# Performance work log

Measured on AMD Instinct MI355X. Metric: run time of the kernel, lower is better.

## Reference

```python
import jax, jax.numpy as jnp
import numpy as np

B, C, D_IN, D_H, D_OUT = 131072, 16, 256, 1024, 256


def setup_inputs() -> dict:
    key = jax.random.key(0)
    k = jax.random.split(key, 6)
    return {
        "x": jax.random.normal(k[0], (B, D_IN), dtype=jnp.float32),
        "cat_ids": jax.random.randint(k[1], (B,), 0, C, dtype=jnp.int32),
        "W1": jax.random.normal(k[2], (C, D_IN, D_H), dtype=jnp.float32) * (1.0 / np.sqrt(D_IN)),
        "b1": jax.random.normal(k[3], (C, D_H), dtype=jnp.float32) * 0.02,
        "W2": jax.random.normal(k[4], (C, D_H, D_OUT), dtype=jnp.float32) * (1.0 / np.sqrt(D_H)),
        "b2": jax.random.normal(k[5], (C, D_OUT), dtype=jnp.float32) * 0.02,
    }


def _routed_linear(x, cat_ids, W, b):
    # Category-routed linear: out[i] = x[i] @ W[cat_ids[i]] + b[cat_ids[i]].
    # Loop over the small fixed category count (not over tokens); each branch
    # is a dense GEMM masked by the routing assignment. This is equivalent to
    # the original gather -> per-category Linear -> scatter/argsort pattern
    # without materializing per-token weight gathers.
    num_categories = W.shape[0]
    out = jnp.zeros((x.shape[0], W.shape[2]), dtype=x.dtype)
    for c in range(num_categories):
        mask = (cat_ids == c)[:, None]
        out = out + jnp.where(mask, x @ W[c] + b[c], jnp.zeros((), x.dtype))
    return out


def reference(x, cat_ids, W1, b1, W2, b2):
    hidden = jax.nn.relu(_routed_linear(x, cat_ids, W1, b1))
    return _routed_linear(hidden, cat_ids, W2, b2)
```

## Files before the change

### kernel.cpp

```cpp
#include <hip/hip_runtime.h>
#include <hip/hip_bf16.h>

#define BB   131072
#define CC   16
#define DIN  256
#define DH   1024
#define DOUT 256
#define TM   128
#define NHB  32
#define NB   512

typedef __attribute__((ext_vector_type(8))) short bf16x8;
typedef __attribute__((ext_vector_type(4))) short short4v;
typedef __attribute__((ext_vector_type(4))) float f32x4;

__device__ inline unsigned short f2b(float f) {
  union { float f; unsigned u; } v; v.f = f;
  unsigned u = v.u;
  return (unsigned short)((u + 0x7fffu + ((u >> 16) & 1u)) >> 16);
}

__device__ inline void gload_lds16(const void* g, void* l) {
  __builtin_amdgcn_global_load_lds(
      (const __attribute__((address_space(1))) void*)g,
      (__attribute__((address_space(3))) void*)l, 16, 0, 0);
}

#define MFMA16(a, b, c) __builtin_amdgcn_mfma_f32_16x16x32_bf16((a), (b), (c), 0, 0, 0)

__global__ void hist_k(const int* __restrict__ cat, int* __restrict__ blockhist) {
  __shared__ int h[CC];
  const int tid = threadIdx.x;
  if (tid < CC) h[tid] = 0;
  __syncthreads();
  const int i = blockIdx.x * 256 + tid;
  atomicAdd(&h[cat[i]], 1);
  __syncthreads();
  if (tid < CC) blockhist[blockIdx.x * CC + tid] = h[tid];
}

__global__ void offsets2_k(const int* __restrict__ blockhist,
                           int* __restrict__ counts, int* __restrict__ padoff,
                           int* __restrict__ base) {
  __shared__ int part[CC][64];
  __shared__ int pref[CC][64];
  __shared__ int scnt[CC];
  __shared__ int spad[CC + 1];
  const int tid = threadIdx.x;
  const int c = tid >> 6;
  const int g = tid & 63;
  int h[8];
  int s = 0;
#pragma unroll
  for (int i = 0; i < 8; i++) {
    h[i] = blockhist[(g * 8 + i) * CC + c];
    s += h[i];
  }
  part[c][g] = s;
  __syncthreads();
  if (g == 0) {
    int r = 0;
    for (int j = 0; j < 64; j++) { pref[c][j] = r; r += part[c][j]; }
    scnt[c] = r;
  }
  __syncthreads();
  if (tid == 0) {
    int acc = 0;
    for (int c2 = 0; c2 < CC; c2++) {
      spad[c2] = acc;
      padoff[c2] = acc;
      counts[c2] = scnt[c2];
      acc += ((scnt[c2] + TM - 1) / TM) * TM;
    }
    spad[CC] = acc;
    padoff[CC] = acc;
  }
  __syncthreads();
  int run = spad[c] + pref[c][g];
#pragma unroll
  for (int i = 0; i < 8; i++) {
    base[(g * 8 + i) * CC + c] = run;
    run += h[i];
  }
}

__global__ void scatter2_k(const int* __restrict__ cat, const int* __restrict__ base,
                           int* __restrict__ idx) {
  __shared__ int cur[CC];
  const int tid = threadIdx.x;
  if (tid < CC) cur[tid] = base[blockIdx.x * CC + tid];
  __syncthreads();
  const int i = blockIdx.x * 256 + tid;
  const int c = cat[i];
  const int pos = atomicAdd(&cur[c], 1);
  idx[pos] = i;
}

__global__ void conv_w1_k(const float* __restrict__ W1, short* __restrict__ w1b) {
  int t = blockIdx.x * blockDim.x + threadIdx.x;
  int n  = t & 1023;
  int j8 = (t >> 10) & 31;
  int c  = t >> 15;
  const float* src = W1 + (size_t)c * DIN * DH;
  bf16x8 o;
#pragma unroll
  for (int i = 0; i < 8; i++)
    o[i] = (short)f2b(src[(size_t)(j8 * 8 + i) * DH + n]);
  char* dst = (char*)w1b + (size_t)c * 524288
            + (n >> 5) * 16384 + ((n >> 4) & 1) * 8192 + (j8 >> 2) * 1024
            + ((n & 15) + 16 * (j8 & 3)) * 16;
  *(bf16x8*)dst = o;
}

__global__ void conv_w2_k(const float* __restrict__ W2, short* __restrict__ w2b) {
  int t = blockIdx.x * blockDim.x + threadIdx.x;
  int n  = t & 255;
  int j8 = (t >> 8) & 127;
  int c  = t >> 15;
  const float* src = W2 + (size_t)c * DH * DOUT;
  bf16x8 o;
#pragma unroll
  for (int i = 0; i < 8; i++)
    o[i] = (short)f2b(src[(size_t)(j8 * 8 + i) * DOUT + n]);
  char* dst = (char*)w2b + (size_t)c * 524288
            + (j8 >> 2) * 16384 + (n >> 4) * 1024
            + ((n & 15) + 16 * (j8 & 3)) * 16;
  *(bf16x8*)dst = o;
}

#define W2OFF  32768
#define HSOFF  65536
#define TKOFF  81920
#define B1OFF  82432
#define B2OFF  86528
#define SMSZ   87552

__launch_bounds__(512, 2)
__global__ void mlp_k(const float* __restrict__ x,
                      const float* __restrict__ b1,
                      const float* __restrict__ b2,
                      const short* __restrict__ w1b,
                      const short* __restrict__ w2b,
                      const int* __restrict__ idx,
                      const int* __restrict__ padoff,
                      const int* __restrict__ counts,
                      float* __restrict__ out) {
  __shared__ __align__(16) char sm[SMSZ];

  const int bhw = blockIdx.x;
  const int wg = (bhw & 7) * 130 + (bhw >> 3);
  const int p = wg * TM;
  const int total = padoff[CC];
  if (p >= total) return;
  int c = 0;
  while (padoff[c + 1] <= p) c++;
  const int cnt = counts[c];
  const int start = p - padoff[c];

  const int tid  = threadIdx.x;
  const int lane = tid & 63;
  const int w    = tid >> 6;
  const int wt   = w >> 1;
  const int wh   = w & 1;
  const int lrow = lane & 15;
  const int lgrp = lane >> 4;

  char*  hsb   = sm + HSOFF;
  int*   toksp = (int*)(sm + TKOFF);
  float* b1s   = (float*)(sm + B1OFF);
  float* b2s   = (float*)(sm + B2OFF);

  {
    const int r = tid >> 2;
    const int q = tid & 3;
    const int pos = start + r;
    int tok = (pos < cnt) ? idx[p + r] : -1;
    if (q == 0) toksp[r] = tok;
    char* tb = sm + (r >> 4) * 8192 + (r & 15) * 16;
    if (tok >= 0) {
      const f32x4* src = (const f32x4*)(x + (size_t)tok * DIN) + q * 16;
#pragma unroll
      for (int t = 0; t < 8; t++) {
        f32x4 v0 = src[2 * t];
        f32x4 v1 = src[2 * t + 1];
        bf16x8 o;
        o[0] = (short)f2b(v0[0]); o[1] = (short)f2b(v0[1]);
        o[2] = (short)f2b(v0[2]); o[3] = (short)f2b(v0[3]);
        o[4] = (short)f2b(v1[0]); o[5] = (short)f2b(v1[1]);
        o[6] = (short)f2b(v1[2]); o[7] = (short)f2b(v1[3]);
        *(bf16x8*)(tb + (2 * q + (t >> 2)) * 1024 + (t & 3) * 256) = o;
      }
    } else {
      bf16x8 z = {0, 0, 0, 0, 0, 0, 0, 0};
#pragma unroll
      for (int t = 0; t < 8; t++)
        *(bf16x8*)(tb + (2 * q + (t >> 2)) * 1024 + (t & 3) * 256) = z;
    }
    if (tid < 256) ((f32x4*)b1s)[tid] = ((const f32x4*)(b1 + (size_t)c * DH))[tid];
    if (tid < 64)  ((f32x4*)b2s)[tid] = ((const f32x4*)(b2 + (size_t)c * DOUT))[tid];
  }
  __syncthreads();

  bf16x8 xf[2][8];
#pragma unroll
  for (int ti = 0; ti < 2; ti++)
#pragma unroll
    for (int ks = 0; ks < 8; ks++)
      xf[ti][ks] = *(const bf16x8*)(sm + (2 * wt + ti) * 8192 + ks * 1024 + lane * 16);
  __syncthreads();

  const char* w1g = (const char*)w1b + (size_t)c * 524288;
  const char* w2g = (const char*)w2b + (size_t)c * 524288;

  auto stage1 = [&](int i) {
    const char* src = w1g + (size_t)i * 16384;
    char* dst = sm + (i & 1) * 16384;
#pragma unroll
    for (int j = 0; j < 2; j++) {
      int chunk = (w * 2 + j) * 1024;
      gload_lds16(src + chunk + lane * 16, dst + chunk);
    }
  };
  auto stage2 = [&](int i) {
    const char* src = w2g + (size_t)i * 16384;
    char* dst = sm + W2OFF + (i & 1) * 16384;
#pragma unroll
    for (int j = 0; j < 2; j++) {
      int chunk = (w * 2 + j) * 1024;
      gload_lds16(src + chunk + lane * 16, dst + chunk);
    }
  };

  f32x4 acc2[2][8];
#pragma unroll
  for (int ti = 0; ti < 2; ti++)
#pragma unroll
    for (int ni = 0; ni < 8; ni++)
      acc2[ti][ni] = (f32x4){0.f, 0.f, 0.f, 0.f};

  const int hswr = (lrow + 16 * (wh * 2 + (lgrp >> 1))) * 16 + (lgrp & 1) * 8;

  stage1(0);
  asm volatile("s_waitcnt vmcnt(0)" ::: "memory");
  __builtin_amdgcn_s_barrier();

  {
    stage2(0);
    stage1(1);
    const char* w1c = sm + wh * 8192;
    f32x4 p0 = (f32x4){0.f, 0.f, 0.f, 0.f};
    f32x4 p1 = (f32x4){0.f, 0.f, 0.f, 0.f};
    __builtin_amdgcn_s_setprio(1);
#pragma unroll
    for (int ks = 0; ks < 8; ks++) {
      bf16x8 a = *(const bf16x8*)(w1c + ks * 1024 + lane * 16);
      p0 = MFMA16(a, xf[0][ks], p0);
      p1 = MFMA16(a, xf[1][ks], p1);
    }
    __builtin_amdgcn_s_setprio(0);
    f32x4 bv = *(const f32x4*)(b1s + wh * 16 + lgrp * 4);
    short4v h0, h1;
#pragma unroll
    for (int jj = 0; jj < 4; jj++) {
      h0[jj] = (short)f2b(fmaxf(p0[jj] + bv[jj], 0.0f));
      h1[jj] = (short)f2b(fmaxf(p1[jj] + bv[jj], 0.0f));
    }
    *(short4v*)(hsb + (2 * wt) * 1024 + hswr)     = h0;
    *(short4v*)(hsb + (2 * wt + 1) * 1024 + hswr) = h1;
    asm volatile("s_waitcnt vmcnt(0) lgkmcnt(0)" ::: "memory");
    __builtin_amdgcn_s_barrier();
  }

  for (int i = 1; i < NHB; i++) {
    stage2(i);
    if (i < NHB - 1) stage1(i + 1);

    const char* hr  = hsb + ((i - 1) & 1) * 8192;
    const char* w2c = sm + W2OFF + ((i - 1) & 1) * 16384;
    const char* w1c = sm + (i & 1) * 16384 + wh * 8192;

    bf16x8 hf0 = *(const bf16x8*)(hr + (2 * wt) * 1024 + lane * 16);
    bf16x8 hf1 = *(const bf16x8*)(hr + (2 * wt + 1) * 1024 + lane * 16);

    __builtin_amdgcn_s_setprio(1);
#pragma unroll
    for (int ni = 0; ni < 8; ni++) {
      bf16x8 a2 = *(const bf16x8*)(w2c + (wh * 8 + ni) * 1024 + lane * 16);
      acc2[0][ni] = MFMA16(a2, hf0, acc2[0][ni]);
      acc2[1][ni] = MFMA16(a2, hf1, acc2[1][ni]);
    }
    f32x4 p0 = (f32x4){0.f, 0.f, 0.f, 0.f};
    f32x4 p1 = (f32x4){0.f, 0.f, 0.f, 0.f};
#pragma unroll
    for (int ks = 0; ks < 8; ks++) {
      bf16x8 a = *(const bf16x8*)(w1c + ks * 1024 + lane * 16);
      p0 = MFMA16(a, xf[0][ks], p0);
      p1 = MFMA16(a, xf[1][ks], p1);
    }
    __builtin_amdgcn_s_setprio(0);

    f32x4 bv = *(const f32x4*)(b1s + i * 32 + wh * 16 + lgrp * 4);
    short4v h0, h1;
#pragma unroll
    for (int jj = 0; jj < 4; jj++) {
      h0[jj] = (short)f2b(fmaxf(p0[jj] + bv[jj], 0.0f));
      h1[jj] = (short)f2b(fmaxf(p1[jj] + bv[jj], 0.0f));
    }
    char* hw = hsb + (i & 1) * 8192;
    *(short4v*)(hw + (2 * wt) * 1024 + hswr)     = h0;
    *(short4v*)(hw + (2 * wt + 1) * 1024 + hswr) = h1;

    asm volatile("s_waitcnt vmcnt(0) lgkmcnt(0)" ::: "memory");
    __builtin_amdgcn_s_barrier();
  }

  {
    const char* hr  = hsb + ((NHB - 1) & 1) * 8192;
    const char* w2c = sm + W2OFF + ((NHB - 1) & 1) * 16384;
    bf16x8 hf0 = *(const bf16x8*)(hr + (2 * wt) * 1024 + lane * 16);
    bf16x8 hf1 = *(const bf16x8*)(hr + (2 * wt + 1) * 1024 + lane * 16);
#pragma unroll
    for (int ni = 0; ni < 8; ni++) {
      bf16x8 a2 = *(const bf16x8*)(w2c + (wh * 8 + ni) * 1024 + lane * 16);
      acc2[0][ni] = MFMA16(a2, hf0, acc2[0][ni]);
      acc2[1][ni] = MFMA16(a2, hf1, acc2[1][ni]);
    }
  }

#pragma unroll
  for (int ti = 0; ti < 2; ti++) {
    const int tok = toksp[(2 * wt + ti) * 16 + lrow];
    if (tok >= 0) {
#pragma unroll
      for (int ni = 0; ni < 8; ni++) {
        const int n0 = (wh * 8 + ni) * 16 + lgrp * 4;
        f32x4 bv = *(const f32x4*)(b2s + n0);
        f32x4 v = acc2[ti][ni] + bv;
        *(f32x4*)(out + (size_t)tok * DOUT + n0) = v;
      }
    }
  }
}

extern "C" void kernel_launch(void* const* d_in, const int* in_sizes, int n_in,
                              void* d_out, int out_size, void* d_ws, size_t ws_size,
                              hipStream_t stream) {
  (void)in_sizes; (void)n_in; (void)out_size; (void)ws_size;
  const float* x   = (const float*)d_in[0];
  const int*   cat = (const int*)d_in[1];
  const float* W1  = (const float*)d_in[2];
  const float* b1  = (const float*)d_in[3];
  const float* W2  = (const float*)d_in[4];
  const float* b2  = (const float*)d_in[5];
  float* out = (float*)d_out;

  char* ws = (char*)d_ws;
  int* counts    = (int*)(ws);
  int* padoff    = (int*)(ws + 128);
  int* blockhist = (int*)(ws + 4096);
  int* base      = (int*)(ws + 65536);
  int* idx       = (int*)(ws + 131072);
  short* w1b     = (short*)(ws + (1 << 20));
  short* w2b     = (short*)(ws + (1 << 20) + 8388608);

  hist_k<<<NB, 256, 0, stream>>>(cat, blockhist);
  offsets2_k<<<1, 1024, 0, stream>>>(blockhist, counts, padoff, base);
  scatter2_k<<<NB, 256, 0, stream>>>(cat, base, idx);
  conv_w1_k<<<2048, 256, 0, stream>>>(W1, w1b);
  conv_w2_k<<<2048, 256, 0, stream>>>(W2, w2b);

  const int ntiles = BB / TM + CC;
  mlp_k<<<ntiles, 512, 0, stream>>>(x, b1, b2, w1b, w2b, idx, padoff, counts, out);
}
```

Measured before the change: 243.7 us.

## Halve token tile to 64 with 256-thread blocks and serialize hidden pipeline

Shrinks the per-workgroup token tile from 128 to 64 rows and the block from 8 to 4 waves, doubling the number of workgroups and shrinking LDS use. The software pipeline is rewritten so both weight slices for the next hidden block are prefetched together, with the hidden activations single-buffered and two barriers per iteration instead of one. The change aims at better occupancy and load balance across CUs. In exchange, each weight byte is reused across half as many tokens and the layer-2 MFMAs no longer overlap the layer-1 MFMAs, so weight traffic and barrier count per token both rise.

```diff
diff --git a/kernel.cpp b/kernel.cpp
--- a/kernel.cpp
+++ b/kernel.cpp
@@ -6,7 +6,7 @@
 #define DIN  256
 #define DH   1024
 #define DOUT 256
-#define TM   128
+#define TM   64
 #define NHB  32
 #define NB   512
 
@@ -130,12 +130,12 @@
 
 #define W2OFF  32768
 #define HSOFF  65536
-#define TKOFF  81920
-#define B1OFF  82432
-#define B2OFF  86528
-#define SMSZ   87552
-
-__launch_bounds__(512, 2)
+#define TKOFF  69632
+#define B1OFF  69888
+#define B2OFF  73984
+#define SMSZ   75008
+
+__launch_bounds__(256, 2)
 __global__ void mlp_k(const float* __restrict__ x,
                       const float* __restrict__ b1,
                       const float* __restrict__ b2,
@@ -148,7 +148,7 @@
   __shared__ __align__(16) char sm[SMSZ];
 
   const int bhw = blockIdx.x;
-  const int wg = (bhw & 7) * 130 + (bhw >> 3);
+  const int wg = (bhw & 7) * 258 + (bhw >> 3);
   const int p = wg * TM;
   const int total = padoff[CC];
   if (p >= total) return;
@@ -196,8 +196,8 @@
       for (int t = 0; t < 8; t++)
         *(bf16x8*)(tb + (2 * q + (t >> 2)) * 1024 + (t & 3) * 256) = z;
     }
-    if (tid < 256) ((f32x4*)b1s)[tid] = ((const f32x4*)(b1 + (size_t)c * DH))[tid];
-    if (tid < 64)  ((f32x4*)b2s)[tid] = ((const f32x4*)(b2 + (size_t)c * DOUT))[tid];
+    ((f32x4*)b1s)[tid] = ((const f32x4*)(b1 + (size_t)c * DH))[tid];
+    if (tid < 64) ((f32x4*)b2s)[tid] = ((const f32x4*)(b2 + (size_t)c * DOUT))[tid];
   }
   __syncthreads();
 
@@ -216,8 +216,8 @@
     const char* src = w1g + (size_t)i * 16384;
     char* dst = sm + (i & 1) * 16384;
 #pragma unroll
-    for (int j = 0; j < 2; j++) {
-      int chunk = (w * 2 + j) * 1024;
+    for (int j = 0; j < 4; j++) {
+      int chunk = (w * 4 + j) * 1024;
       gload_lds16(src + chunk + lane * 16, dst + chunk);
     }
   };
@@ -225,11 +225,16 @@
     const char* src = w2g + (size_t)i * 16384;
     char* dst = sm + W2OFF + (i & 1) * 16384;
 #pragma unroll
-    for (int j = 0; j < 2; j++) {
-      int chunk = (w * 2 + j) * 1024;
+    for (int j = 0; j < 4; j++) {
+      int chunk = (w * 4 + j) * 1024;
       gload_lds16(src + chunk + lane * 16, dst + chunk);
     }
   };
+
+  stage1(0);
+  stage2(0);
+  asm volatile("s_waitcnt vmcnt(0)" ::: "memory");
+  __syncthreads();
 
   f32x4 acc2[2][8];
 #pragma unroll
@@ -240,14 +245,13 @@
 
   const int hswr = (lrow + 16 * (wh * 2 + (lgrp >> 1))) * 16 + (lgrp & 1) * 8;
 
-  stage1(0);
-  asm volatile("s_waitcnt vmcnt(0)" ::: "memory");
-  __builtin_amdgcn_s_barrier();
-
-  {
-    stage2(0);
-    stage1(1);
-    const char* w1c = sm + wh * 8192;
+  for (int hb = 0; hb < NHB; hb++) {
+    const char* w1c = sm + (hb & 1) * 16384 + wh * 8192;
+    const char* w2c = sm + W2OFF + (hb & 1) * 16384;
+    const bool notlast = (hb < NHB - 1);
+
+    if (notlast) { stage1(hb + 1); stage2(hb + 1); }
+
     f32x4 p0 = (f32x4){0.f, 0.f, 0.f, 0.f};
     f32x4 p1 = (f32x4){0.f, 0.f, 0.f, 0.f};
     __builtin_amdgcn_s_setprio(1);
@@ -258,72 +262,39 @@
       p1 = MFMA16(a, xf[1][ks], p1);
     }
     __builtin_amdgcn_s_setprio(0);
-    f32x4 bv = *(const f32x4*)(b1s + wh * 16 + lgrp * 4);
-    short4v h0, h1;
-#pragma unroll
-    for (int jj = 0; jj < 4; jj++) {
-      h0[jj] = (short)f2b(fmaxf(p0[jj] + bv[jj], 0.0f));
-      h1[jj] = (short)f2b(fmaxf(p1[jj] + bv[jj], 0.0f));
-    }
-    *(short4v*)(hsb + (2 * wt) * 1024 + hswr)     = h0;
-    *(short4v*)(hsb + (2 * wt + 1) * 1024 + hswr) = h1;
-    asm volatile("s_waitcnt vmcnt(0) lgkmcnt(0)" ::: "memory");
+
+    {
+      f32x4 bv = *(const f32x4*)(b1s + hb * 32 + wh * 16 + lgrp * 4);
+      short4v h0, h1;
+#pragma unroll
+      for (int jj = 0; jj < 4; jj++) {
+        h0[jj] = (short)f2b(fmaxf(p0[jj] + bv[jj], 0.0f));
+        h1[jj] = (short)f2b(fmaxf(p1[jj] + bv[jj], 0.0f));
+      }
+      *(short4v*)(hsb + (2 * wt) * 1024 + hswr)     = h0;
+      *(short4v*)(hsb + (2 * wt + 1) * 1024 + hswr) = h1;
+    }
+    if (notlast)
+      asm volatile("s_waitcnt vmcnt(8) lgkmcnt(0)" ::: "memory");
+    else
+      asm volatile("s_waitcnt vmcnt(0) lgkmcnt(0)" ::: "memory");
     __builtin_amdgcn_s_barrier();
-  }
-
-  for (int i = 1; i < NHB; i++) {
-    stage2(i);
-    if (i < NHB - 1) stage1(i + 1);
-
-    const char* hr  = hsb + ((i - 1) & 1) * 8192;
-    const char* w2c = sm + W2OFF + ((i - 1) & 1) * 16384;
-    const char* w1c = sm + (i & 1) * 16384 + wh * 8192;
-
-    bf16x8 hf0 = *(const bf16x8*)(hr + (2 * wt) * 1024 + lane * 16);
-    bf16x8 hf1 = *(const bf16x8*)(hr + (2 * wt + 1) * 1024 + lane * 16);
-
-    __builtin_amdgcn_s_setprio(1);
-#pragma unroll
-    for (int ni = 0; ni < 8; ni++) {
-      bf16x8 a2 = *(const bf16x8*)(w2c + (wh * 8 + ni) * 1024 + lane * 16);
-      acc2[0][ni] = MFMA16(a2, hf0, acc2[0][ni]);
-      acc2[1][ni] = MFMA16(a2, hf1, acc2[1][ni]);
-    }
-    f32x4 p0 = (f32x4){0.f, 0.f, 0.f, 0.f};
-    f32x4 p1 = (f32x4){0.f, 0.f, 0.f, 0.f};
-#pragma unroll
-    for (int ks = 0; ks < 8; ks++) {
-      bf16x8 a = *(const bf16x8*)(w1c + ks * 1024 + lane * 16);
-      p0 = MFMA16(a, xf[0][ks], p0);
-      p1 = MFMA16(a, xf[1][ks], p1);
-    }
-    __builtin_amdgcn_s_setprio(0);
-
-    f32x4 bv = *(const f32x4*)(b1s + i * 32 + wh * 16 + lgrp * 4);
-    short4v h0, h1;
-#pragma unroll
-    for (int jj = 0; jj < 4; jj++) {
-      h0[jj] = (short)f2b(fmaxf(p0[jj] + bv[jj], 0.0f));
-      h1[jj] = (short)f2b(fmaxf(p1[jj] + bv[jj], 0.0f));
-    }
-    char* hw = hsb + (i & 1) * 8192;
-    *(short4v*)(hw + (2 * wt) * 1024 + hswr)     = h0;
-    *(short4v*)(hw + (2 * wt + 1) * 1024 + hswr) = h1;
-
-    asm volatile("s_waitcnt vmcnt(0) lgkmcnt(0)" ::: "memory");
-    __builtin_amdgcn_s_barrier();
-  }
-
-  {
-    const char* hr  = hsb + ((NHB - 1) & 1) * 8192;
-    const char* w2c = sm + W2OFF + ((NHB - 1) & 1) * 16384;
-    bf16x8 hf0 = *(const bf16x8*)(hr + (2 * wt) * 1024 + lane * 16);
-    bf16x8 hf1 = *(const bf16x8*)(hr + (2 * wt + 1) * 1024 + lane * 16);
-#pragma unroll
-    for (int ni = 0; ni < 8; ni++) {
-      bf16x8 a2 = *(const bf16x8*)(w2c + (wh * 8 + ni) * 1024 + lane * 16);
-      acc2[0][ni] = MFMA16(a2, hf0, acc2[0][ni]);
-      acc2[1][ni] = MFMA16(a2, hf1, acc2[1][ni]);
+
+    {
+      bf16x8 hf0 = *(const bf16x8*)(hsb + (2 * wt) * 1024 + lane * 16);
+      bf16x8 hf1 = *(const bf16x8*)(hsb + (2 * wt + 1) * 1024 + lane * 16);
+      __builtin_amdgcn_s_setprio(1);
+#pragma unroll
+      for (int ni = 0; ni < 8; ni++) {
+        bf16x8 a2 = *(const bf16x8*)(w2c + (wh * 8 + ni) * 1024 + lane * 16);
+        acc2[0][ni] = MFMA16(a2, hf0, acc2[0][ni]);
+        acc2[1][ni] = MFMA16(a2, hf1, acc2[1][ni]);
+      }
+      __builtin_amdgcn_s_setprio(0);
+    }
+    if (notlast) {
+      asm volatile("s_waitcnt vmcnt(4) lgkmcnt(0)" ::: "memory");
+      __builtin_amdgcn_s_barrier();
     }
   }
 
@@ -333,7 +304,7 @@
     if (tok >= 0) {
 #pragma unroll
       for (int ni = 0; ni < 8; ni++) {
-        const int n0 = (wh * 8 + ni) * 16 + lgrp * 4;
+        const int n0 = wh * 128 + ni * 16 + lgrp * 4;
         f32x4 bv = *(const f32x4*)(b2s + n0);
         f32x4 v = acc2[ti][ni] + bv;
         *(f32x4*)(out + (size_t)tok * DOUT + n0) = v;
@@ -370,5 +341,5 @@
   conv_w2_k<<<2048, 256, 0, stream>>>(W2, w2b);
 
   const int ntiles = BB / TM + CC;
-  mlp_k<<<ntiles, 512, 0, stream>>>(x, b1, b2, w1b, w2b, idx, padoff, counts, out);
-}
+  mlp_k<<<ntiles, 256, 0, stream>>>(x, b1, b2, w1b, w2b, idx, padoff, counts, out);
+}
```

Result: no change. 247.8 us (+1.7%).
